# Optimization experiments

Measured on AMD Instinct MI355X. Metric: run time of the kernel, lower is better.

The kernel has to match this reference:

```python
import jax, jax.numpy as jnp
import numpy as np
import math

B, T, IN_DIM = 2, 2048, 512
D, NH, MULT, N_LAYER = 512, 8, 4, 3
N = D * MULT // NH  # per-head latent dim = 256
OUT_DIM = 512
THETA = 2 ** 16


def get_freqs(n):
    t = jnp.arange(n, dtype=jnp.float32)
    q = jnp.floor(t / 2.0) * 2.0  # quantize(q=2)
    return 1.0 / (THETA ** (q / n)) / (2.0 * math.pi)


def ln(x, eps=1e-5):
    mu = jnp.mean(x, axis=-1, keepdims=True)
    var = jnp.var(x, axis=-1, keepdims=True)
    return (x - mu) * jax.lax.rsqrt(var + eps)


def rope(phases, v):
    # phases: [T, N] broadcastable to v [B, nh, T, N]
    p = (phases % 1.0) * (2.0 * math.pi)
    pc, ps = jnp.cos(p), jnp.sin(p)
    # interleave rotate: out[..., 2i] = -v[..., 2i+1], out[..., 2i+1] = v[..., 2i]
    v_rot = jnp.stack((-v[..., 1::2], v[..., ::2]), axis=-1).reshape(v.shape)
    return v * pc + v_rot * ps


def setup_inputs() -> dict:
    key = jax.random.key(0)
    ks = jax.random.split(key, 8)
    std = 0.02
    return {
        "x": jax.random.normal(ks[0], (B, T, IN_DIM), dtype=jnp.float32),
        "w_in": jax.random.normal(ks[1], (IN_DIM, D), dtype=jnp.float32) * std,
        "b_in": jnp.zeros((D,), dtype=jnp.float32),
        "encoder": jax.random.normal(ks[2], (NH, D, N), dtype=jnp.float32) * std,
        "encoder_v": jax.random.normal(ks[3], (NH, D, N), dtype=jnp.float32) * std,
        "decoder": jax.random.normal(ks[4], (NH * N, D), dtype=jnp.float32) * std,
        "head_w": jax.random.normal(ks[5], (D, OUT_DIM), dtype=jnp.float32) * std,
        "head_b": jnp.zeros((OUT_DIM,), dtype=jnp.float32),
    }


def reference(x, w_in, b_in, encoder, encoder_v, decoder, head_w, head_b):
    freqs = get_freqs(N)  # [N]
    t_idx = jnp.arange(T, dtype=jnp.float32)
    phases = t_idx[:, None] * freqs[None, :]  # [T, N]
    # strict lower-triangular causal mask (tril diagonal=-1)
    mask = (jnp.arange(T)[:, None] > jnp.arange(T)[None, :])  # [T, T]
    dec = decoder.reshape(NH, N, D)

    xs = ln(x @ w_in + b_in)  # [B, T, D]
    for _ in range(N_LAYER):
        x_res = xs
        x_sparse = jax.nn.relu(jnp.einsum('btd,hdn->bhtn', xs, encoder))  # [B,nh,T,N]
        QR = rope(phases, x_sparse)
        scores = jnp.einsum('bhtn,bhsn->bhts', QR, QR)
        scores = jnp.where(mask, scores, 0.0)
        yKV = jnp.einsum('bhts,bsd->bhtd', scores, xs)  # V = x (head-broadcast)
        yKV = ln(yKV)
        y_sparse = jax.nn.relu(jnp.einsum('bhtd,hdn->bhtn', yKV, encoder_v))
        xy_sparse = x_sparse * y_sparse  # dropout p=0 -> identity
        yMLP = jnp.einsum('bhtn,hnd->btd', xy_sparse, dec)
        xs = ln(x_res + ln(yMLP))
    logits = xs @ head_w + head_b
    return logits
```

## Files before the change

### kernel.cpp

```cpp
#include <hip/hip_runtime.h>
#include <math.h>

constexpr int B_  = 2;
constexpr int T_  = 2048;
constexpr int D_  = 512;
constexpr int NH_ = 8;
constexpr int NL_ = 256;
constexpr int HN_ = NH_ * NL_;
constexpr int BT_ = B_ * T_;

typedef __bf16 v8bf __attribute__((ext_vector_type(8)));
typedef float  v4f  __attribute__((ext_vector_type(4)));
typedef unsigned short us8 __attribute__((ext_vector_type(8)));
typedef unsigned short us4 __attribute__((ext_vector_type(4)));

__device__ inline unsigned short f2b(float f) {
    union { float f; unsigned u; } v{f};
    unsigned r = v.u + 0x7FFF + ((v.u >> 16) & 1);
    return (unsigned short)(r >> 16);
}
__device__ inline float b2f(unsigned short u) {
    union { unsigned u; float f; } v{(unsigned)u << 16};
    return v.f;
}

__device__ __forceinline__ void g2l16(const void* g, void* l) {
    __builtin_amdgcn_global_load_lds(
        (const __attribute__((address_space(1))) void*)g,
        (__attribute__((address_space(3))) void*)l, 16, 0, 0);
}

#define TILE_IDS                                              \
    int tid = threadIdx.x;                                    \
    int lane = tid & 63, wid = tid >> 6;                      \
    int wm = (wid & 1) * 64, wn = (wid >> 1) * 64;            \
    int ln16 = lane & 15, q = lane >> 4;                      \
    int srl = lane >> 2, scl = (lane & 3) * 8;                \
    (void)wm; (void)wn;

#define T128_STAGE(Ab, lda, Bb, ldb, k0, buf)                 \
    _Pragma("unroll")                                         \
    for (int ci = 0; ci < 4; ++ci) {                          \
        int c = wid * 4 + ci;                                 \
        if (c < 8) {                                          \
            int r = c * 16 + srl;                             \
            g2l16(Ab + (long)r * lda + (k0) + scl,            \
                  (char*)As[buf] + c * 1024);                 \
        } else {                                              \
            int r = (c - 8) * 16 + srl;                       \
            g2l16(Bb + (long)r * ldb + (k0) + scl,            \
                  (char*)Bs[buf] + (c - 8) * 1024);           \
        }                                                     \
    }

#define TILE_MFMA(Asx, Bsx)                                   \
    {                                                         \
        v8bf af[4], bfr[4];                                   \
        _Pragma("unroll")                                     \
        for (int r = 0; r < 4; ++r)                           \
            af[r] = *(const v8bf*)&Asx[wm + r * 16 + ln16][q * 8]; \
        _Pragma("unroll")                                     \
        for (int c = 0; c < 4; ++c)                           \
            bfr[c] = *(const v8bf*)&Bsx[wn + c * 16 + ln16][q * 8]; \
        _Pragma("unroll")                                     \
        for (int r = 0; r < 4; ++r)                           \
            _Pragma("unroll")                                 \
            for (int c = 0; c < 4; ++c)                       \
                acc[r][c] = __builtin_amdgcn_mfma_f32_16x16x32_bf16( \
                    af[r], bfr[c], acc[r][c], 0, 0, 0);       \
    }

template <int KS, bool RELU, bool MUL, bool BF16OUT, bool LNA>
__global__ __launch_bounds__(256) void gemm128(
    const unsigned short* __restrict__ A, int lda, long sA,
    const unsigned short* __restrict__ Bt, int ldb, long sB,
    void* __restrict__ Cv, int ldc, long sC,
    const unsigned short* __restrict__ mulp, int K,
    const float* __restrict__ muinv, const float* __restrict__ colsum) {
    constexpr int NHF = KS / 32;
    int m0 = blockIdx.y * 128, n0 = blockIdx.x * 128, z = blockIdx.z;
    __shared__ unsigned short As[2][NHF][128][32];
    __shared__ unsigned short Bs[2][NHF][128][32];
    const unsigned short* Ab = A  + (long)z * sA + (long)m0 * lda;
    const unsigned short* Bb = Bt + (long)z * sB + (long)n0 * ldb;
    TILE_IDS
    v4f acc[4][4] = {};
    auto stageK = [&](int k0, int buf) {
        #pragma unroll
        for (int h = 0; h < NHF; ++h)
            #pragma unroll
            for (int ci = 0; ci < 4; ++ci) {
                int c = wid * 4 + ci;
                if (c < 8)
                    g2l16(Ab + (long)(c * 16 + srl) * lda + k0 + h * 32 + scl,
                          (char*)As[buf][h] + c * 1024);
                else
                    g2l16(Bb + (long)((c - 8) * 16 + srl) * ldb + k0 + h * 32 +
                              scl,
                          (char*)Bs[buf][h] + (c - 8) * 1024);
            }
    };
    stageK(0, 0);
    __syncthreads();
    int cur = 0;
    for (int k0 = 0; k0 < K; k0 += KS) {
        if (k0 + KS < K) stageK(k0 + KS, cur ^ 1);
        #pragma unroll
        for (int h = 0; h < NHF; ++h)
            TILE_MFMA(As[cur][h], Bs[cur][h])
        __syncthreads();
        cur ^= 1;
    }
    float* Cf = (float*)Cv;
    unsigned short* Cb = (unsigned short*)Cv;
    long zoff = (long)z * sC;
    #pragma unroll
    for (int r = 0; r < 4; ++r)
        #pragma unroll
        for (int c = 0; c < 4; ++c)
            #pragma unroll
            for (int e = 0; e < 4; ++e) {
                int row = m0 + wm + r * 16 + q * 4 + e;
                int col = n0 + wn + c * 16 + ln16;
                float v = acc[r][c][e];
                if (LNA) {
                    float2 mi = *(const float2*)&muinv[((long)z * BT_ + row) * 2];
                    float cs = colsum[(long)z * NL_ + col];
                    v = mi.y * (v - mi.x * cs);
                }
                if (RELU) v = fmaxf(v, 0.f);
                long idx = zoff + (long)row * ldc + col;
                if (MUL) v *= b2f(mulp[idx]);
                if (BF16OUT) Cb[idx] = f2b(v);
                else         Cf[idx] = v;
            }
}

__global__ __launch_bounds__(256) void enc_rope(
    const unsigned short* __restrict__ A,
    const unsigned short* __restrict__ Bt,
    unsigned short* __restrict__ xsp,
    unsigned short* __restrict__ qrh,
    unsigned short* __restrict__ qrT) {
    int m0 = blockIdx.y * 128, n0 = blockIdx.x * 128;
    __shared__ unsigned short As[2][2][128][32];
    __shared__ unsigned short Bs[2][2][128][32];
    unsigned short (*lt)[68] = (unsigned short(*)[68])&As[0][0][0][0];
    const unsigned short* Ab = A + (long)m0 * 512;
    const unsigned short* Bb = Bt + (long)n0 * 512;
    TILE_IDS
    v4f acc[4][4] = {};
    auto stageK = [&](int k0, int buf) {
        #pragma unroll
        for (int h = 0; h < 2; ++h)
            #pragma unroll
            for (int ci = 0; ci < 4; ++ci) {
                int c = wid * 4 + ci;
                if (c < 8)
                    g2l16(Ab + (long)(c * 16 + srl) * 512 + k0 + h * 32 + scl,
                          (char*)As[buf][h] + c * 1024);
                else
                    g2l16(Bb + (long)((c - 8) * 16 + srl) * 512 + k0 + h * 32 +
                              scl,
                          (char*)Bs[buf][h] + (c - 8) * 1024);
            }
    };
    stageK(0, 0);
    __syncthreads();
    int cur = 0;
    for (int k0 = 0; k0 < 512; k0 += 64) {
        if (k0 + 64 < 512) stageK(k0 + 64, cur ^ 1);
        TILE_MFMA(As[cur][0], Bs[cur][0])
        TILE_MFMA(As[cur][1], Bs[cur][1])
        __syncthreads();
        cur ^= 1;
    }
    int bb = m0 >> 11;
    int tbase = m0 & (T_ - 1);
    #pragma unroll
    for (int half = 0; half < 2; ++half) {
        if (wm == half * 64) {
            #pragma unroll
            for (int r = 0; r < 4; ++r)
                #pragma unroll
                for (int c = 0; c < 4; ++c)
                    #pragma unroll
                    for (int e = 0; e < 4; ++e) {
                        int rl = wm + r * 16 + q * 4 + e;
                        int col = n0 + wn + c * 16 + ln16;
                        float v = fmaxf(acc[r][c][e], 0.f);
                        xsp[(long)(m0 + rl) * HN_ + col] = f2b(v);
                        int n = col & (NL_ - 1);
                        int n2 = n >> 1;
                        float fr = exp2f(-(float)n2 * 0.125f) *
                                   (float)(1.0 / (2.0 * M_PI));
                        float ph = (float)(tbase + rl) * fr;
                        ph = (ph - floorf(ph)) * (float)(2.0 * M_PI);
                        float s, cc;
                        __sincosf(ph, &s, &cc);
                        float vp = __shfl_xor(v, 1, 64);
                        float o = (n & 1) ? (v * cc + vp * s)
                                          : (v * cc - vp * s);
                        int hh = col >> 8;
                        qrh[((long)(bb * 8 + hh) * T_ + tbase + rl) * NL_ + n] =
                            f2b(o);
                        lt[wn + c * 16 + ln16][rl & 63] = f2b(o);
                    }
        }
        __syncthreads();
        {
            int nrow = tid >> 1, tseg = (tid & 1) * 32;
            int colg = n0 + nrow;
            int hh = colg >> 8, nn = colg & (NL_ - 1);
            long ob = ((long)(bb * 8 + hh) * NL_ + nn) * T_ + tbase +
                      half * 64 + tseg;
            #pragma unroll
            for (int u = 0; u < 8; ++u)
                *(us4*)&qrT[ob + u * 4] = *(const us4*)&lt[nrow][tseg + u * 4];
        }
        __syncthreads();
    }
}

__global__ __launch_bounds__(256) void ct_gemm(
    const unsigned short* __restrict__ xsT,
    const unsigned short* __restrict__ qrT,
    unsigned short* __restrict__ Ct) {
    int z = blockIdx.x, nt = blockIdx.y;
    int j = blockIdx.z >> 2, mt = blockIdx.z & 3;
    int b = z >> 3;
    const unsigned short* Ab =
        xsT + (long)b * D_ * T_ + (long)(mt * 128) * T_ + j * 256;
    const unsigned short* Bb =
        qrT + (long)z * NL_ * T_ + (long)(nt * 128) * T_ + j * 256;
    __shared__ unsigned short As[2][128][32];
    __shared__ unsigned short Bs[2][128][32];
    TILE_IDS
    v4f acc[4][4] = {};
    T128_STAGE(Ab, T_, Bb, T_, 0, 0)
    __syncthreads();
    int cur = 0;
    for (int k0 = 0; k0 < 256; k0 += 32) {
        if (k0 + 32 < 256) { T128_STAGE(Ab, T_, Bb, T_, k0 + 32, cur ^ 1) }
        TILE_MFMA(As[cur], Bs[cur])
        __syncthreads();
        cur ^= 1;
    }
    unsigned short* ob = Ct + ((long)z * 8 + j) * 512 * 256;
    #pragma unroll
    for (int r = 0; r < 4; ++r)
        #pragma unroll
        for (int c = 0; c < 4; ++c)
            #pragma unroll
            for (int e = 0; e < 4; ++e) {
                int row = mt * 128 + wm + r * 16 + q * 4 + e;
                int col = nt * 128 + wn + c * 16 + ln16;
                ob[(long)row * 256 + col] = f2b(acc[r][c][e]);
            }
}

__global__ __launch_bounds__(256) void prefix_k(unsigned short* __restrict__ Ct) {
    int z = blockIdx.x, dg = blockIdx.y;
    int d = dg * 8 + (threadIdx.x >> 5);
    int n0 = (threadIdx.x & 31) * 8;
    long base = ((long)z * 8) * 512 * 256 + (long)d * 256 + n0;
    constexpr long S = 512 * 256;
    us8 vals[8];
    #pragma unroll
    for (int i = 0; i < 8; ++i)
        vals[i] = *(const us8*)&Ct[base + (long)i * S];
    float acc[8] = {};
    #pragma unroll
    for (int i = 0; i < 8; ++i) {
        us8 o;
        #pragma unroll
        for (int e = 0; e < 8; ++e) o[e] = f2b(acc[e]);
        *(us8*)&Ct[base + (long)i * S] = o;
        #pragma unroll
        for (int e = 0; e < 8; ++e) acc[e] += b2f(vals[i][e]);
    }
}

__global__ __launch_bounds__(256) void sdiag(const unsigned short* __restrict__ qr,
                                             unsigned short* __restrict__ Sd) {
    int z = blockIdx.x, i = blockIdx.y, qq = blockIdx.z;
    int qm = (qq + 1) >> 1, qn = qq >> 1;
    const unsigned short* Ab =
        qr + ((long)z * T_ + i * 256 + qm * 128) * NL_;
    const unsigned short* Bb =
        qr + ((long)z * T_ + i * 256 + qn * 128) * NL_;
    bool dual = (qm != qn);
    __shared__ unsigned short As[2][128][32];
    __shared__ unsigned short Bs[2][128][32];
    TILE_IDS
    v4f acc[4][4] = {};
    auto stg = [&](int k0, int buf) {
        #pragma unroll
        for (int ci = 0; ci < 2; ++ci) {
            int c = wid * 2 + ci;
            g2l16(Ab + (long)(c * 16 + srl) * NL_ + k0 + scl,
                  (char*)As[buf] + c * 1024);
            if (dual)
                g2l16(Bb + (long)(c * 16 + srl) * NL_ + k0 + scl,
                      (char*)Bs[buf] + c * 1024);
        }
    };
    stg(0, 0);
    __syncthreads();
    int cur = 0;
    for (int k0 = 0; k0 < NL_; k0 += 32) {
        if (k0 + 32 < NL_) stg(k0 + 32, cur ^ 1);
        if (dual) { TILE_MFMA(As[cur], Bs[cur]) }
        else      { TILE_MFMA(As[cur], As[cur]) }
        __syncthreads();
        cur ^= 1;
    }
    unsigned short* ob = Sd + ((long)z * 8 + i) * 65536;
    #pragma unroll
    for (int r = 0; r < 4; ++r)
        #pragma unroll
        for (int c = 0; c < 4; ++c)
            #pragma unroll
            for (int e = 0; e < 4; ++e) {
                int row = wm + r * 16 + q * 4 + e;
                int col = wn + c * 16 + ln16;
                float v = acc[r][c][e];
                if (!dual && row <= col) v = 0.f;
                ob[(qm * 128 + row) * 256 + qn * 128 + col] = f2b(v);
            }
}

__global__ __launch_bounds__(256) void pxg(
    const unsigned short* __restrict__ qr,
    const unsigned short* __restrict__ Pt,
    const unsigned short* __restrict__ Sd,
    const unsigned short* __restrict__ xsT,
    unsigned short* __restrict__ ykvu,
    float* __restrict__ part) {
    int z = blockIdx.x, i = blockIdx.y, nt = blockIdx.z;
    int b = z >> 3, h = z & 7;
    int n0 = nt * 128;
    int i256 = i >> 1, hf2 = i & 1;
    const unsigned short* A1 = qr + ((long)z * T_ + i * 128) * NL_;
    const unsigned short* B1 =
        Pt + ((long)z * 8 + i256) * 512 * 256 + (long)n0 * 256;
    const unsigned short* A2 = Sd + ((long)z * 8 + i256) * 65536 +
                               (long)hf2 * 128 * 256;
    const unsigned short* B2 =
        xsT + (long)b * D_ * T_ + (long)n0 * T_ + i256 * 256;
    __shared__ unsigned short As[2][128][32];
    __shared__ unsigned short Bs[2][128][32];
    __shared__ float sred[128][2][2];
    TILE_IDS
    v4f acc[4][4] = {};
    int NS = 12 + hf2 * 4;
    auto stage = [&](int s) {
        const unsigned short* Ap;
        const unsigned short* Bp;
        long lda, ldb;
        int k0;
        if (s < 8) { Ap = A1; lda = NL_; Bp = B1; ldb = 256; k0 = s * 32; }
        else       { Ap = A2; lda = 256; Bp = B2; ldb = T_;  k0 = (s - 8) * 32; }
        int bi = s & 1;
        #pragma unroll
        for (int ci = 0; ci < 4; ++ci) {
            int c = wid * 4 + ci;
            if (c < 8)
                g2l16(Ap + (long)(c * 16 + srl) * lda + k0 + scl,
                      (char*)As[bi] + c * 1024);
            else
                g2l16(Bp + (long)((c - 8) * 16 + srl) * ldb + k0 + scl,
                      (char*)Bs[bi] + (c - 8) * 1024);
        }
    };
    stage(0);
    __syncthreads();
    for (int s = 0; s < NS; ++s) {
        if (s + 1 < NS) stage(s + 1);
        int bi = s & 1;
        TILE_MFMA(As[bi], Bs[bi])
        __syncthreads();
    }
    long obase = ((long)h * BT_ + (long)b * T_ + i * 128) * D_ + n0;
    #pragma unroll
    for (int r = 0; r < 4; ++r) {
        float s1[4] = {}, s2[4] = {};
        #pragma unroll
        for (int c = 0; c < 4; ++c)
            #pragma unroll
            for (int e = 0; e < 4; ++e) {
                float v = acc[r][c][e];
                s1[e] += v;
                s2[e] += v * v;
                int rl = wm + r * 16 + q * 4 + e;
                int col = wn + c * 16 + ln16;
                ykvu[obase + (long)rl * D_ + col] = f2b(v);
            }
        #pragma unroll
        for (int e = 0; e < 4; ++e) {
            #pragma unroll
            for (int off = 1; off < 16; off <<= 1) {
                s1[e] += __shfl_xor(s1[e], off, 64);
                s2[e] += __shfl_xor(s2[e], off, 64);
            }
            if (ln16 == 0) {
                int rl = wm + r * 16 + q * 4 + e;
                sred[rl][wid >> 1][0] = s1[e];
                sred[rl][wid >> 1][1] = s2[e];
            }
        }
    }
    __syncthreads();
    if (tid < 128) {
        float a = sred[tid][0][0] + sred[tid][1][0];
        float sq = sred[tid][0][1] + sred[tid][1][1];
        long pb = ((((long)z * 16 + i) * 4 + nt) * 128 + tid) * 2;
        part[pb] = a;
        part[pb + 1] = sq;
    }
}

__global__ __launch_bounds__(128) void lnstats(const float* __restrict__ part,
                                               float* __restrict__ muinv) {
    int z = blockIdx.x, i = blockIdx.y, t = threadIdx.x;
    long pb = ((((long)z * 16 + i) * 4) * 128 + t) * 2;
    float s1 = part[pb] + part[pb + 256] + part[pb + 512] + part[pb + 768];
    float s2 = part[pb + 1] + part[pb + 257] + part[pb + 513] + part[pb + 769];
    float mu = s1 * (1.0f / 512.0f);
    float var = s2 * (1.0f / 512.0f) - mu * mu;
    float inv = rsqrtf(var + 1e-5f);
    int b = z >> 3, h = z & 7;
    long row = (long)h * BT_ + (long)b * T_ + i * 128 + t;
    muinv[row * 2]     = mu;
    muinv[row * 2 + 1] = inv;
}

__global__ __launch_bounds__(256) void colsum_k(
    const unsigned short* __restrict__ encvT, float* __restrict__ cs) {
    int lane = threadIdx.x & 63, wv = threadIdx.x >> 6;
    int g = blockIdx.x * 4 + wv;
    us8 v = *(const us8*)&encvT[(long)g * 512 + lane * 8];
    float s = 0.f;
    #pragma unroll
    for (int e = 0; e < 8; ++e) s += b2f(v[e]);
    #pragma unroll
    for (int off = 1; off < 64; off <<= 1) s += __shfl_xor(s, off, 64);
    if (lane == 0) cs[g] = s;
}

__global__ __launch_bounds__(256) void trans_cast(
    const float* __restrict__ in, long sIn, unsigned short* __restrict__ out,
    long sOut, int R, int Cc) {
    __shared__ float tl[32][33];
    int z = blockIdx.z;
    int r0 = blockIdx.y * 32, c0 = blockIdx.x * 32;
    int tx = threadIdx.x & 31, ty = threadIdx.x >> 5;
    const float* ip = in + (long)z * sIn;
    unsigned short* op = out + (long)z * sOut;
    #pragma unroll
    for (int j = 0; j < 4; ++j)
        tl[ty + j * 8][tx] = ip[(long)(r0 + ty + j * 8) * Cc + c0 + tx];
    __syncthreads();
    #pragma unroll
    for (int j = 0; j < 4; ++j)
        op[(long)(c0 + ty + j * 8) * R + r0 + tx] = f2b(tl[tx][ty + j * 8]);
}

__global__ __launch_bounds__(256) void cast_b(const float* __restrict__ in,
                                              unsigned short* __restrict__ out) {
    long i = ((long)blockIdx.x * 256 + threadIdx.x) * 4;
    float4 v = *(const float4*)&in[i];
    ushort4 o;
    o.x = f2b(v.x); o.y = f2b(v.y); o.z = f2b(v.z); o.w = f2b(v.w);
    *(ushort4*)&out[i] = o;
}

__global__ __launch_bounds__(256) void add_out4(const float* __restrict__ t,
                                                long slice,
                                                const float* __restrict__ bias,
                                                float* __restrict__ o) {
    long i = ((long)blockIdx.x * 256 + threadIdx.x) * 4;
    float4 v0 = *(const float4*)&t[i];
    float4 v1 = *(const float4*)&t[i + slice];
    float4 v2 = *(const float4*)&t[i + 2 * slice];
    float4 v3 = *(const float4*)&t[i + 3 * slice];
    float4 bv = *(const float4*)&bias[i & 511];
    float4 r;
    r.x = v0.x + v1.x + v2.x + v3.x + bv.x;
    r.y = v0.y + v1.y + v2.y + v3.y + bv.y;
    r.z = v0.z + v1.z + v2.z + v3.z + bv.z;
    r.w = v0.w + v1.w + v2.w + v3.w + bv.w;
    *(float4*)&o[i] = r;
}

__device__ inline float2 block_reduce2(float a, float b) {
    __shared__ float sa[4], sb[4];
    #pragma unroll
    for (int off = 32; off; off >>= 1) {
        a += __shfl_down(a, off, 64);
        b += __shfl_down(b, off, 64);
    }
    __syncthreads();
    int w = threadIdx.x >> 6;
    if ((threadIdx.x & 63) == 0) { sa[w] = a; sb[w] = b; }
    __syncthreads();
    return make_float2(sa[0] + sa[1] + sa[2] + sa[3],
                       sb[0] + sb[1] + sb[2] + sb[3]);
}
__device__ inline float2 ln_pair(float2 v) {
    float2 s = block_reduce2(v.x + v.y, 0.f);
    float mu = s.x * (1.0f / 512.0f);
    float dx = v.x - mu, dy = v.y - mu;
    float2 q = block_reduce2(dx * dx + dy * dy, 0.f);
    float inv = rsqrtf(q.x * (1.0f / 512.0f) + 1e-5f);
    return make_float2(dx * inv, dy * inv);
}

__global__ __launch_bounds__(256) void ln_dual4(const float* __restrict__ t,
                                                long slice,
                                                const float* __restrict__ bias,
                                                float* __restrict__ outf,
                                                unsigned short* __restrict__ outb) {
    long row = blockIdx.x;
    int c = threadIdx.x * 2;
    long i = row * 512 + c;
    float2 v0 = *(const float2*)&t[i];
    float2 v1 = *(const float2*)&t[i + slice];
    float2 v2 = *(const float2*)&t[i + 2 * slice];
    float2 v3 = *(const float2*)&t[i + 3 * slice];
    float2 bv = *(const float2*)&bias[c];
    float2 v = make_float2(v0.x + v1.x + v2.x + v3.x + bv.x,
                           v0.y + v1.y + v2.y + v3.y + bv.y);
    float2 o = ln_pair(v);
    *(float2*)&outf[i] = o;
    ushort2 ob; ob.x = f2b(o.x); ob.y = f2b(o.y);
    *(ushort2*)&outb[i] = ob;
}

__global__ __launch_bounds__(256) void combine_dual4(
    const float* __restrict__ t, long slice, const float* __restrict__ xres,
    float* __restrict__ outf, unsigned short* __restrict__ outb) {
    long row = blockIdx.x;
    int c = threadIdx.x * 2;
    long i = row * 512 + c;
    float2 v0 = *(const float2*)&t[i];
    float2 v1 = *(const float2*)&t[i + slice];
    float2 v2 = *(const float2*)&t[i + 2 * slice];
    float2 v3 = *(const float2*)&t[i + 3 * slice];
    float2 y = make_float2(v0.x + v1.x + v2.x + v3.x,
                           v0.y + v1.y + v2.y + v3.y);
    float2 l = ln_pair(y);
    float2 r = *(const float2*)&xres[i];
    float2 z = make_float2(r.x + l.x, r.y + l.y);
    float2 o = ln_pair(z);
    *(float2*)&outf[i] = o;
    ushort2 ob; ob.x = f2b(o.x); ob.y = f2b(o.y);
    *(ushort2*)&outb[i] = ob;
}

extern "C" void kernel_launch(void* const* d_in, const int* in_sizes, int n_in,
                              void* d_out, int out_size, void* d_ws,
                              size_t ws_size, hipStream_t stream) {
    const float* x      = (const float*)d_in[0];
    const float* w_in   = (const float*)d_in[1];
    const float* b_in   = (const float*)d_in[2];
    const float* enc    = (const float*)d_in[3];
    const float* enc_v  = (const float*)d_in[4];
    const float* dec    = (const float*)d_in[5];
    const float* head_w = (const float*)d_in[6];
    const float* head_b = (const float*)d_in[7];
    float* out = (float*)d_out;

    char* w = (char*)d_ws;
    auto alloc = [&](size_t bytes) { void* p = (void*)w; w += bytes; return p; };
    unsigned short* w_inT = (unsigned short*)alloc((size_t)512 * 512 * 2);
    unsigned short* headT = (unsigned short*)alloc((size_t)512 * 512 * 2);
    unsigned short* encT  = (unsigned short*)alloc((size_t)NH_ * NL_ * D_ * 2);
    unsigned short* encvT = (unsigned short*)alloc((size_t)NH_ * NL_ * D_ * 2);
    unsigned short* decT  = (unsigned short*)alloc((size_t)D_ * HN_ * 2);
    unsigned short* xb    = (unsigned short*)alloc((size_t)BT_ * D_ * 2);
    float*          tmp   = (float*)alloc((size_t)4 * BT_ * D_ * 4);
    float*          xsf0  = (float*)alloc((size_t)BT_ * D_ * 4);
    float*          xsf1  = (float*)alloc((size_t)BT_ * D_ * 4);
    unsigned short* xs_b  = (unsigned short*)alloc((size_t)BT_ * D_ * 2);
    unsigned short* xsT   = (unsigned short*)alloc((size_t)B_ * D_ * T_ * 2);
    unsigned short* xsp   = (unsigned short*)alloc((size_t)BT_ * HN_ * 2);
    unsigned short* qrh   = (unsigned short*)alloc((size_t)BT_ * HN_ * 2);
    unsigned short* qrT   = (unsigned short*)alloc((size_t)BT_ * HN_ * 2);
    unsigned short* Ct    = (unsigned short*)alloc((size_t)128 * 512 * 256 * 2);
    unsigned short* Sd    = (unsigned short*)alloc((size_t)128 * 256 * 256 * 2);
    unsigned short* ykv   = (unsigned short*)alloc((size_t)NH_ * BT_ * D_ * 2);
    float*          part  = (float*)alloc((size_t)256 * 4 * 128 * 2 * 4);
    float*          muinv = (float*)alloc((size_t)NH_ * BT_ * 2 * 4);
    float*          csum  = (float*)alloc((size_t)HN_ * 4);
    const long SL = (long)BT_ * D_;

    cast_b<<<BT_ * D_ / 1024, 256, 0, stream>>>(x, xb);
    trans_cast<<<dim3(16, 16, 1), 256, 0, stream>>>(w_in, 0, w_inT, 0, 512, 512);
    trans_cast<<<dim3(16, 16, 1), 256, 0, stream>>>(head_w, 0, headT, 0, 512, 512);
    trans_cast<<<dim3(8, 16, 8), 256, 0, stream>>>(enc, (long)D_ * NL_, encT,
                                                   (long)NL_ * D_, D_, NL_);
    trans_cast<<<dim3(8, 16, 8), 256, 0, stream>>>(enc_v, (long)D_ * NL_, encvT,
                                                   (long)NL_ * D_, D_, NL_);
    trans_cast<<<dim3(16, 64, 1), 256, 0, stream>>>(dec, 0, decT, 0, HN_, D_);
    colsum_k<<<HN_ / 4, 256, 0, stream>>>(encvT, csum);

    gemm128<64, false, false, false, false>
        <<<dim3(4, 32, 4), 256, 0, stream>>>(xb, D_, 128, w_inT, D_, 128, tmp,
                                             D_, SL, nullptr, 128, nullptr,
                                             nullptr);
    ln_dual4<<<BT_, 256, 0, stream>>>(tmp, SL, b_in, xsf0, xs_b);
    trans_cast<<<dim3(16, 64, 2), 256, 0, stream>>>(xsf0, (long)T_ * D_, xsT,
                                                    (long)D_ * T_, T_, D_);

    float* xin = xsf0;
    float* xout = xsf1;
    for (int l = 0; l < 3; ++l) {
        enc_rope<<<dim3(16, 32), 256, 0, stream>>>(xs_b, encT, xsp, qrh, qrT);
        ct_gemm<<<dim3(16, 2, 32), 256, 0, stream>>>(xsT, qrT, Ct);
        prefix_k<<<dim3(16, 64), 256, 0, stream>>>(Ct);
        sdiag<<<dim3(16, 8, 3), 256, 0, stream>>>(qrh, Sd);
        pxg<<<dim3(16, 16, 4), 256, 0, stream>>>(qrh, Ct, Sd, xsT, ykv, part);
        lnstats<<<dim3(16, 16), 128, 0, stream>>>(part, muinv);
        gemm128<64, true, true, true, true>
            <<<dim3(2, 32, 8), 256, 0, stream>>>(
                ykv, D_, (long)BT_ * D_, encvT, D_, (long)NL_ * D_, xsp, HN_,
                NL_, xsp, 512, muinv, csum);
        gemm128<64, false, false, false, false>
            <<<dim3(4, 32, 4), 256, 0, stream>>>(
                xsp, HN_, 512, decT, HN_, 512, tmp, D_, SL, nullptr, 512,
                nullptr, nullptr);
        combine_dual4<<<BT_, 256, 0, stream>>>(tmp, SL, xin, xout, xs_b);
        trans_cast<<<dim3(16, 64, 2), 256, 0, stream>>>(xout, (long)T_ * D_,
                                                        xsT, (long)D_ * T_, T_,
                                                        D_);
        float* t = xin; xin = xout; xout = t;
    }

    gemm128<64, false, false, false, false>
        <<<dim3(4, 32, 4), 256, 0, stream>>>(xs_b, D_, 128, headT, D_, 128, tmp,
                                             D_, SL, nullptr, 128, nullptr,
                                             nullptr);
    add_out4<<<BT_ * 512 / 1024, 256, 0, stream>>>(tmp, SL, head_b, out);
}
```

Baseline: 588.7 us.

## Narrow enc_rope N-tile to 64 and transpose bf16 activations directly

The enc_rope kernel now uses 128x64 output tiles instead of 128x128. This doubles the grid to 1024 blocks, and the qrT transpose is staged in one pass through shared memory rather than two halves. The per-layer activation transpose now reads the bf16 copy instead of the fp32 one, through a new trans16 kernel, which halves the bytes it reads. The smaller tile increases occupancy but reloads the A operand twice as often. The bf16 source keeps the same values, since trans_cast already rounded to bf16.

```diff
diff --git a/kernel.cpp b/kernel.cpp
--- a/kernel.cpp
+++ b/kernel.cpp
@@ -142,20 +142,24 @@
     unsigned short* __restrict__ xsp,
     unsigned short* __restrict__ qrh,
     unsigned short* __restrict__ qrT) {
-    int m0 = blockIdx.y * 128, n0 = blockIdx.x * 128;
+    int m0 = blockIdx.y * 128, n0 = blockIdx.x * 64;
     __shared__ unsigned short As[2][2][128][32];
-    __shared__ unsigned short Bs[2][2][128][32];
-    unsigned short (*lt)[68] = (unsigned short(*)[68])&As[0][0][0][0];
+    __shared__ unsigned short Bs[2][2][64][32];
+    unsigned short (*lt)[132] = (unsigned short(*)[132])&As[0][0][0][0];
     const unsigned short* Ab = A + (long)m0 * 512;
     const unsigned short* Bb = Bt + (long)n0 * 512;
-    TILE_IDS
-    v4f acc[4][4] = {};
+    int tid = threadIdx.x;
+    int lane = tid & 63, wid = tid >> 6;
+    int wm = (wid & 1) * 64, wn2 = (wid >> 1) * 32;
+    int ln16 = lane & 15, q = lane >> 4;
+    int srl = lane >> 2, scl = (lane & 3) * 8;
+    v4f acc[4][2] = {};
     auto stageK = [&](int k0, int buf) {
         #pragma unroll
         for (int h = 0; h < 2; ++h)
             #pragma unroll
-            for (int ci = 0; ci < 4; ++ci) {
-                int c = wid * 4 + ci;
+            for (int ci = 0; ci < 3; ++ci) {
+                int c = wid * 3 + ci;
                 if (c < 8)
                     g2l16(Ab + (long)(c * 16 + srl) * 512 + k0 + h * 32 + scl,
                           (char*)As[buf][h] + c * 1024);
@@ -165,60 +169,66 @@
                           (char*)Bs[buf][h] + (c - 8) * 1024);
             }
     };
+    auto mstep = [&](int buf, int h) {
+        v8bf af[4], bf2[2];
+        #pragma unroll
+        for (int r = 0; r < 4; ++r)
+            af[r] = *(const v8bf*)&As[buf][h][wm + r * 16 + ln16][q * 8];
+        #pragma unroll
+        for (int c = 0; c < 2; ++c)
+            bf2[c] = *(const v8bf*)&Bs[buf][h][wn2 + c * 16 + ln16][q * 8];
+        #pragma unroll
+        for (int r = 0; r < 4; ++r)
+            #pragma unroll
+            for (int c = 0; c < 2; ++c)
+                acc[r][c] = __builtin_amdgcn_mfma_f32_16x16x32_bf16(
+                    af[r], bf2[c], acc[r][c], 0, 0, 0);
+    };
     stageK(0, 0);
     __syncthreads();
     int cur = 0;
     for (int k0 = 0; k0 < 512; k0 += 64) {
         if (k0 + 64 < 512) stageK(k0 + 64, cur ^ 1);
-        TILE_MFMA(As[cur][0], Bs[cur][0])
-        TILE_MFMA(As[cur][1], Bs[cur][1])
+        mstep(cur, 0);
+        mstep(cur, 1);
         __syncthreads();
         cur ^= 1;
     }
     int bb = m0 >> 11;
     int tbase = m0 & (T_ - 1);
     #pragma unroll
-    for (int half = 0; half < 2; ++half) {
-        if (wm == half * 64) {
-            #pragma unroll
-            for (int r = 0; r < 4; ++r)
-                #pragma unroll
-                for (int c = 0; c < 4; ++c)
-                    #pragma unroll
-                    for (int e = 0; e < 4; ++e) {
-                        int rl = wm + r * 16 + q * 4 + e;
-                        int col = n0 + wn + c * 16 + ln16;
-                        float v = fmaxf(acc[r][c][e], 0.f);
-                        xsp[(long)(m0 + rl) * HN_ + col] = f2b(v);
-                        int n = col & (NL_ - 1);
-                        int n2 = n >> 1;
-                        float fr = exp2f(-(float)n2 * 0.125f) *
-                                   (float)(1.0 / (2.0 * M_PI));
-                        float ph = (float)(tbase + rl) * fr;
-                        ph = (ph - floorf(ph)) * (float)(2.0 * M_PI);
-                        float s, cc;
-                        __sincosf(ph, &s, &cc);
-                        float vp = __shfl_xor(v, 1, 64);
-                        float o = (n & 1) ? (v * cc + vp * s)
-                                          : (v * cc - vp * s);
-                        int hh = col >> 8;
-                        qrh[((long)(bb * 8 + hh) * T_ + tbase + rl) * NL_ + n] =
-                            f2b(o);
-                        lt[wn + c * 16 + ln16][rl & 63] = f2b(o);
-                    }
-        }
-        __syncthreads();
-        {
-            int nrow = tid >> 1, tseg = (tid & 1) * 32;
-            int colg = n0 + nrow;
-            int hh = colg >> 8, nn = colg & (NL_ - 1);
-            long ob = ((long)(bb * 8 + hh) * NL_ + nn) * T_ + tbase +
-                      half * 64 + tseg;
-            #pragma unroll
-            for (int u = 0; u < 8; ++u)
-                *(us4*)&qrT[ob + u * 4] = *(const us4*)&lt[nrow][tseg + u * 4];
-        }
-        __syncthreads();
+    for (int r = 0; r < 4; ++r)
+        #pragma unroll
+        for (int c = 0; c < 2; ++c)
+            #pragma unroll
+            for (int e = 0; e < 4; ++e) {
+                int rl = wm + r * 16 + q * 4 + e;
+                int col = n0 + wn2 + c * 16 + ln16;
+                float v = fmaxf(acc[r][c][e], 0.f);
+                xsp[(long)(m0 + rl) * HN_ + col] = f2b(v);
+                int n = col & (NL_ - 1);
+                int n2 = n >> 1;
+                float fr = exp2f(-(float)n2 * 0.125f) *
+                           (float)(1.0 / (2.0 * M_PI));
+                float ph = (float)(tbase + rl) * fr;
+                ph = (ph - floorf(ph)) * (float)(2.0 * M_PI);
+                float s, cc;
+                __sincosf(ph, &s, &cc);
+                float vp = __shfl_xor(v, 1, 64);
+                float o = (n & 1) ? (v * cc + vp * s) : (v * cc - vp * s);
+                int hh = col >> 8;
+                qrh[((long)(bb * 8 + hh) * T_ + tbase + rl) * NL_ + n] = f2b(o);
+                lt[wn2 + c * 16 + ln16][rl] = f2b(o);
+            }
+    __syncthreads();
+    {
+        int nrow = tid >> 2, tseg = (tid & 3) * 32;
+        int colg = n0 + nrow;
+        int hh = colg >> 8, nn = colg & (NL_ - 1);
+        long ob = ((long)(bb * 8 + hh) * NL_ + nn) * T_ + tbase + tseg;
+        #pragma unroll
+        for (int u = 0; u < 8; ++u)
+            *(us4*)&qrT[ob + u * 4] = *(const us4*)&lt[nrow][tseg + u * 4];
     }
 }
 
@@ -466,6 +476,24 @@
         op[(long)(c0 + ty + j * 8) * R + r0 + tx] = f2b(tl[tx][ty + j * 8]);
 }
 
+__global__ __launch_bounds__(256) void trans16(
+    const unsigned short* __restrict__ in, long sIn,
+    unsigned short* __restrict__ out, long sOut, int R, int Cc) {
+    __shared__ unsigned short tl[32][34];
+    int z = blockIdx.z;
+    int r0 = blockIdx.y * 32, c0 = blockIdx.x * 32;
+    int tx = threadIdx.x & 31, ty = threadIdx.x >> 5;
+    const unsigned short* ip = in + (long)z * sIn;
+    unsigned short* op = out + (long)z * sOut;
+    #pragma unroll
+    for (int j = 0; j < 4; ++j)
+        tl[ty + j * 8][tx] = ip[(long)(r0 + ty + j * 8) * Cc + c0 + tx];
+    __syncthreads();
+    #pragma unroll
+    for (int j = 0; j < 4; ++j)
+        op[(long)(c0 + ty + j * 8) * R + r0 + tx] = tl[tx][ty + j * 8];
+}
+
 __global__ __launch_bounds__(256) void cast_b(const float* __restrict__ in,
                                               unsigned short* __restrict__ out) {
     long i = ((long)blockIdx.x * 256 + threadIdx.x) * 4;
@@ -610,13 +638,13 @@
                                              D_, SL, nullptr, 128, nullptr,
                                              nullptr);
     ln_dual4<<<BT_, 256, 0, stream>>>(tmp, SL, b_in, xsf0, xs_b);
-    trans_cast<<<dim3(16, 64, 2), 256, 0, stream>>>(xsf0, (long)T_ * D_, xsT,
-                                                    (long)D_ * T_, T_, D_);
+    trans16<<<dim3(16, 64, 2), 256, 0, stream>>>(xs_b, (long)T_ * D_, xsT,
+                                                 (long)D_ * T_, T_, D_);
 
     float* xin = xsf0;
     float* xout = xsf1;
     for (int l = 0; l < 3; ++l) {
-        enc_rope<<<dim3(16, 32), 256, 0, stream>>>(xs_b, encT, xsp, qrh, qrT);
+        enc_rope<<<dim3(32, 32), 256, 0, stream>>>(xs_b, encT, xsp, qrh, qrT);
         ct_gemm<<<dim3(16, 2, 32), 256, 0, stream>>>(xsT, qrT, Ct);
         prefix_k<<<dim3(16, 64), 256, 0, stream>>>(Ct);
         sdiag<<<dim3(16, 8, 3), 256, 0, stream>>>(qrh, Sd);
@@ -631,9 +659,8 @@
                 xsp, HN_, 512, decT, HN_, 512, tmp, D_, SL, nullptr, 512,
                 nullptr, nullptr);
         combine_dual4<<<BT_, 256, 0, stream>>>(tmp, SL, xin, xout, xs_b);
-        trans_cast<<<dim3(16, 64, 2), 256, 0, stream>>>(xout, (long)T_ * D_,
-                                                        xsT, (long)D_ * T_, T_,
-                                                        D_);
+        trans16<<<dim3(16, 64, 2), 256, 0, stream>>>(xs_b, (long)T_ * D_, xsT,
+                                                     (long)D_ * T_, T_, D_);
         float* t = xin; xin = xout; xout = t;
     }
 
```

Result: slower. 600.9 us (+2.1%).
